# Kernel tuning notes

Hardware: AMD Instinct MI355X
Metric: run time of the kernel (lower is better)

Reference implementation:

```python
import jax, jax.numpy as jnp
import numpy as np

B, T, D = 2, 2048, 1024
H, RANK = 16, 32
DH = D // H  # 64


def setup_inputs() -> dict:
    key = jax.random.key(0)
    ks = jax.random.split(key, 6)
    sd = 1.0 / np.sqrt(D)
    sdh = 1.0 / np.sqrt(DH)
    return {
        "x": jax.random.normal(ks[0], (B, T, D), dtype=jnp.float32),
        "W_qkv": jax.random.normal(ks[1], (D, 3 * D), dtype=jnp.float32) * sd,
        "W_q_lsr": jax.random.normal(ks[2], (H, DH, RANK), dtype=jnp.float32) * sdh,
        "W_k_lsr": jax.random.normal(ks[3], (H, DH, RANK), dtype=jnp.float32) * sdh,
        "lsr_core": jnp.ones((H, RANK), dtype=jnp.float32),
        "W_o": jax.random.normal(ks[4], (D, D), dtype=jnp.float32) * sd,
    }


def reference(x, W_qkv, W_q_lsr, W_k_lsr, lsr_core, W_o):
    b, t, d = x.shape
    # Fused QKV projection
    qkv = x @ W_qkv  # (B, T, 3D)
    q, k, v = jnp.split(qkv, 3, axis=-1)
    # (B, H, T, DH)
    q = q.reshape(b, t, H, DH).transpose(0, 2, 1, 3)
    k = k.reshape(b, t, H, DH).transpose(0, 2, 1, 3)
    v = v.reshape(b, t, H, DH).transpose(0, 2, 1, 3)
    # Low-rank bilinear score: q^T Wq diag(core) Wk^T k
    ql = jnp.einsum("bhtd,hdr->bhtr", q, W_q_lsr)  # (B, H, T, R)
    kl = jnp.einsum("bhsd,hdr->bhsr", k, W_k_lsr)  # (B, H, T, R)
    scale = 1.0 / jnp.sqrt(jnp.asarray(RANK, dtype=x.dtype))
    scores = jnp.einsum("bhtr,bhsr->bhts", ql * lsr_core[None, :, None, :], kl) * scale
    # Causal mask
    causal = jnp.tril(jnp.ones((t, t), dtype=bool))
    scores = jnp.where(causal[None, None], scores, jnp.asarray(-jnp.inf, dtype=scores.dtype))
    attn = jax.nn.softmax(scores, axis=-1)
    y = jnp.einsum("bhts,bhsd->bhtd", attn, v)  # (B, H, T, DH)
    y = y.transpose(0, 2, 1, 3).reshape(b, t, d)
    return y @ W_o
```

## Files before the change

### kernel.cpp

```cpp
#include <hip/hip_runtime.h>
#include <hip/hip_bf16.h>

#define B_  2
#define T_  2048
#define D_  1024
#define H_  16
#define DH_ 64
#define R_  32
#define BT_ (B_*T_)
#define BH_ (B_*H_)

typedef unsigned short u16;
typedef unsigned int   u32;
typedef __attribute__((ext_vector_type(8))) short bhalf8;
typedef __attribute__((ext_vector_type(4))) float floatx4;

#define WSB_FLAG  0
#define WSB_XB    256
#define WSB_WCATT (WSB_XB    + 8388608)
#define WSB_QL    (WSB_WCATT + 4194304)
#define WSB_KL    (WSB_QL    + 4194304)
#define WSB_VT    (WSB_KL    + 4194304)
#define WSB_YB    (WSB_VT    + 8388608)
#define WSB_WOT   (WSB_YB    + 8388608)

#define NEG_ -1.0e30f

__device__ __forceinline__ float bfs(u16 s) {
    union { u32 i; float f; } w; w.i = ((u32)s) << 16; return w.f;
}
__device__ __forceinline__ u16 tob(float f) {
    __hip_bfloat16 h = __float2bfloat16(f);
    return *(u16*)&h;
}
__device__ __forceinline__ u32 pack2(float a, float b) {
    return (u32)tob(a) | ((u32)tob(b) << 16);
}
__device__ __forceinline__ void gload16(const u16* g, u16* l) {
    __builtin_amdgcn_global_load_lds(
        (const __attribute__((address_space(1))) void*)g,
        (__attribute__((address_space(3))) void*)l, 16, 0, 0);
}
__device__ __forceinline__ int detect_isbf(const u32* __restrict__ xw, int lane) {
    int hits = 0;
    #pragma unroll
    for (int i = 0; i < 8; ++i) {
        const u32 w = xw[lane + i * 64];
        const u32 h = w & 0xFFFFu;
        const u32 e = (h >> 7) & 0xFFu;
        if (h == 0u || (e >= 100u && e <= 150u)) ++hits;
    }
    #pragma unroll
    for (int off = 32; off; off >>= 1) hits += __shfl_down(hits, off, 64);
    return __shfl(hits, 0, 64) >= 300;
}

__global__ __launch_bounds__(256) void prep_kernel(
    const void* __restrict__ x, u16* __restrict__ xb,
    const void* __restrict__ Wqkv, const void* __restrict__ Wo,
    const void* __restrict__ Wq_lsr, const void* __restrict__ Wk_lsr,
    const void* __restrict__ core,
    u16* __restrict__ WcatT, u16* __restrict__ WoT)
{
    __shared__ __align__(16) u16 Bq[128 * 72];
    __shared__ __align__(16) u16 Bk[128 * 72];
    __shared__ __align__(16) u16 Aq[32 * 72];
    __shared__ __align__(16) u16 Ak[32 * 72];
    const int tid  = threadIdx.x;
    const int lane = tid & 63;
    const int isbf = detect_isbf((const u32*)x, lane);
    const int blk  = blockIdx.x;
    const int w    = tid >> 6;
    const int n16  = lane & 15;
    const int q4   = lane >> 4;

    if (blk < 2048) {
        const int e = blk * 256 + tid;
        if (isbf) {
            ((uint4*)xb)[e] = ((const uint4*)x)[e];
        } else {
            float4 a0 = ((const float4*)x)[2*e];
            float4 a1 = ((const float4*)x)[2*e + 1];
            uint4 o;
            o.x = pack2(a0.x, a0.y); o.y = pack2(a0.z, a0.w);
            o.z = pack2(a1.x, a1.y); o.w = pack2(a1.z, a1.w);
            ((uint4*)xb)[e] = o;
        }
        return;
    }

    if (blk < 2560) {
        int t = blk - 2048;
        const void* src; u16* dst; int srcStride, srcColOff, dstRowOff;
        if (t < 256) { src = Wqkv; dst = WcatT; srcStride = 3*D_; srcColOff = 2*D_; dstRowOff = 1024; }
        else { t -= 256; src = Wo; dst = WoT; srcStride = D_; srcColOff = 0; dstRowOff = 0; }
        const int j0 = (t & 15) * 64;
        const int i0 = (t >> 4) * 64;
        #pragma unroll
        for (int p = 0; p < 2; ++p) {
            const int e = tid + p * 256;
            const int r = e >> 3, ch = e & 7;
            if (isbf) {
                uint4 v = *(const uint4*)((const u16*)src + (size_t)(i0 + r) * srcStride + srcColOff + j0 + ch*8);
                *(uint4*)&Bq[r * 72 + ch*8] = v;
            } else {
                const float* s = (const float*)src + (size_t)(i0 + r) * srcStride + srcColOff + j0 + ch*8;
                float4 a0 = *(const float4*)s;
                float4 a1 = *(const float4*)(s + 4);
                uint4 o;
                o.x = pack2(a0.x, a0.y); o.y = pack2(a0.z, a0.w);
                o.z = pack2(a1.x, a1.y); o.w = pack2(a1.z, a1.w);
                *(uint4*)&Bq[r * 72 + ch*8] = o;
            }
        }
        __syncthreads();
        #pragma unroll
        for (int p = 0; p < 2; ++p) {
            const int e = tid + p * 256;
            const int c = e >> 3, ch = e & 7;
            u16 tmp[8];
            #pragma unroll
            for (int j = 0; j < 8; ++j) tmp[j] = Bq[(ch*8 + j) * 72 + c];
            *(uint4*)(dst + (size_t)(dstRowOff + j0 + c) * D_ + i0 + ch*8) = *(uint4*)tmp;
        }
        return;
    }

    const int fb = blk - 2560;
    const int h  = fb & 15;
    const int d0 = (fb >> 4) * 128;

    #pragma unroll
    for (int p = 0; p < 8; ++p) {
        const int e  = tid + p * 256;
        const int r  = e & 31, dh = e >> 5;
        float aq, ak;
        if (isbf) {
            aq = bfs(((const u16*)Wq_lsr)[(h*DH_ + dh)*R_ + r]);
            ak = bfs(((const u16*)Wk_lsr)[(h*DH_ + dh)*R_ + r]);
        } else {
            aq = ((const float*)Wq_lsr)[(h*DH_ + dh)*R_ + r];
            ak = ((const float*)Wk_lsr)[(h*DH_ + dh)*R_ + r];
        }
        Aq[r * 72 + dh] = tob(aq);
        Ak[r * 72 + dh] = tob(ak);
    }
    #pragma unroll
    for (int p = 0; p < 8; ++p) {
        const int e  = tid + p * 256;
        const int n  = e >> 4, ch = e & 15;
        if (isbf) {
            uint2 wq = *(const uint2*)((const u16*)Wqkv + (size_t)(d0+n)*(3*D_) + h*DH_ + ch*4);
            uint2 wk = *(const uint2*)((const u16*)Wqkv + (size_t)(d0+n)*(3*D_) + D_ + h*DH_ + ch*4);
            *(uint2*)&Bq[n * 72 + ch*4] = wq;
            *(uint2*)&Bk[n * 72 + ch*4] = wk;
        } else {
            float4 fq = *(const float4*)((const float*)Wqkv + (size_t)(d0+n)*(3*D_) + h*DH_ + ch*4);
            float4 fk = *(const float4*)((const float*)Wqkv + (size_t)(d0+n)*(3*D_) + D_ + h*DH_ + ch*4);
            uint2 oq, ok;
            oq.x = pack2(fq.x, fq.y); oq.y = pack2(fq.z, fq.w);
            ok.x = pack2(fk.x, fk.y); ok.y = pack2(fk.z, fk.w);
            *(uint2*)&Bq[n * 72 + ch*4] = oq;
            *(uint2*)&Bk[n * 72 + ch*4] = ok;
        }
    }
    __syncthreads();

    floatx4 accq[2][2], acck[2][2];
    #pragma unroll
    for (int mi = 0; mi < 2; ++mi)
        #pragma unroll
        for (int ni = 0; ni < 2; ++ni) { accq[mi][ni] = (floatx4)(0.f); acck[mi][ni] = (floatx4)(0.f); }

    #pragma unroll
    for (int kk = 0; kk < 2; ++kk) {
        bhalf8 aqf[2], akf[2], bqf[2], bkf[2];
        #pragma unroll
        for (int mi = 0; mi < 2; ++mi) {
            aqf[mi] = *(const bhalf8*)&Aq[(mi*16 + n16) * 72 + kk*32 + q4*8];
            akf[mi] = *(const bhalf8*)&Ak[(mi*16 + n16) * 72 + kk*32 + q4*8];
        }
        #pragma unroll
        for (int ni = 0; ni < 2; ++ni) {
            bqf[ni] = *(const bhalf8*)&Bq[(w*32 + ni*16 + n16) * 72 + kk*32 + q4*8];
            bkf[ni] = *(const bhalf8*)&Bk[(w*32 + ni*16 + n16) * 72 + kk*32 + q4*8];
        }
        #pragma unroll
        for (int mi = 0; mi < 2; ++mi)
            #pragma unroll
            for (int ni = 0; ni < 2; ++ni) {
                accq[mi][ni] = __builtin_amdgcn_mfma_f32_16x16x32_bf16(aqf[mi], bqf[ni], accq[mi][ni], 0, 0, 0);
                acck[mi][ni] = __builtin_amdgcn_mfma_f32_16x16x32_bf16(akf[mi], bkf[ni], acck[mi][ni], 0, 0, 0);
            }
    }

    const float scale = (float)(0.17677669529663687 * 1.4426950408889634);
    #pragma unroll
    for (int mi = 0; mi < 2; ++mi) {
        #pragma unroll
        for (int rr = 0; rr < 4; ++rr) {
            const int r = mi*16 + q4*4 + rr;
            const float cc = (isbf ? bfs(((const u16*)core)[h*R_ + r])
                                   : ((const float*)core)[h*R_ + r]) * scale;
            #pragma unroll
            for (int ni = 0; ni < 2; ++ni) {
                const int d = d0 + w*32 + ni*16 + n16;
                WcatT[(size_t)(h*R_ + r) * D_ + d]       = tob(accq[mi][ni][rr] * cc);
                WcatT[(size_t)(512 + h*R_ + r) * D_ + d] = tob(acck[mi][ni][rr]);
            }
        }
    }
}

__global__ __launch_bounds__(256, 4) void gemm1_mfma(
    const u16* __restrict__ xb, const u16* __restrict__ WcatT,
    u16* __restrict__ ql, u16* __restrict__ kl, u16* __restrict__ vf)
{
    __shared__ __align__(16) u16 As[128 * 64];
    __shared__ __align__(16) u16 Bs[64 * 64];
    const int tid  = threadIdx.x;
    const int lane = tid & 63;
    const int w    = tid >> 6;
    const int n16  = lane & 15;
    const int q4   = lane >> 4;
    const int wx   = w & 1;
    const int wy   = w >> 1;
    const int bm   = blockIdx.y * 128;
    const int bn   = blockIdx.x * 64;
    const int lrow = lane >> 3;
    const int lcol = (lane & 7) * 8;

    floatx4 acc[4][2];
    #pragma unroll
    for (int i = 0; i < 4; ++i)
        #pragma unroll
        for (int j = 0; j < 2; ++j) acc[i][j] = (floatx4)(0.f);

    for (int kt = 0; kt < D_; kt += 64) {
        #pragma unroll
        for (int i = 0; i < 4; ++i) {
            const int r0 = w*32 + i*8;
            gload16(xb + (size_t)(bm + r0 + lrow) * D_ + kt + lcol, &As[r0 * 64]);
        }
        #pragma unroll
        for (int i = 0; i < 2; ++i) {
            const int r0 = w*16 + i*8;
            gload16(WcatT + (size_t)(bn + r0 + lrow) * D_ + kt + lcol, &Bs[r0 * 64]);
        }
        __syncthreads();
        #pragma unroll
        for (int kk = 0; kk < 2; ++kk) {
            bhalf8 a[4], b[2];
            #pragma unroll
            for (int mi = 0; mi < 4; ++mi)
                a[mi] = *(const bhalf8*)&As[(wy*64 + mi*16 + n16) * 64 + kk*32 + q4*8];
            #pragma unroll
            for (int ni = 0; ni < 2; ++ni)
                b[ni] = *(const bhalf8*)&Bs[(wx*32 + ni*16 + n16) * 64 + kk*32 + q4*8];
            #pragma unroll
            for (int mi = 0; mi < 4; ++mi)
                #pragma unroll
                for (int ni = 0; ni < 2; ++ni)
                    acc[mi][ni] = __builtin_amdgcn_mfma_f32_16x16x32_bf16(
                        a[mi], b[ni], acc[mi][ni], 0, 0, 0);
        }
        __syncthreads();
    }

    if (bn < 1024) {
        #pragma unroll
        for (int mi = 0; mi < 4; ++mi) {
            #pragma unroll
            for (int rr = 0; rr < 4; ++rr) {
                const int row = bm + wy*64 + mi*16 + q4*4 + rr;
                const int b   = row >> 11;
                const int t   = row & (T_ - 1);
                #pragma unroll
                for (int ni = 0; ni < 2; ++ni) {
                    const int col = bn + wx*32 + ni*16 + n16;
                    const u16 val = tob(acc[mi][ni][rr]);
                    if (col < 512) {
                        const int h = col >> 5, r = col & 31;
                        ql[((size_t)(b*H_ + h)*T_ + t)*R_ + r] = val;
                    } else {
                        const int c = col - 512; const int h = c >> 5, r = c & 31;
                        kl[((size_t)(b*H_ + h)*T_ + t)*R_ + r] = val;
                    }
                }
            }
        }
    } else {
        #pragma unroll
        for (int mi = 0; mi < 4; ++mi) {
            const int row0 = bm + wy*64 + mi*16 + q4*4;
            const int b  = row0 >> 11;
            const int t  = row0 & (T_ - 1);
            const int tile = t >> 7;
            const int sl   = t & 127;
            const int kc   = sl >> 5;
            const int j2   = (sl >> 4) & 1;
            const int qv   = (sl >> 2) & 3;
            #pragma unroll
            for (int ni = 0; ni < 2; ++ni) {
                const int c  = bn - 1024 + wx*32 + ni*16 + n16;
                const int h  = c >> 6, dh = c & 63;
                const int bh = b*H_ + h;
                const int c2 = dh >> 4;
                const int lv = qv*16 + (dh & 15);
                u16* dst = vf + ((((size_t)bh*16 + tile)*4 + kc)*4 + c2)*512
                              + lv*8 + j2*4;
                uint2 o;
                o.x = pack2(acc[mi][ni][0], acc[mi][ni][1]);
                o.y = pack2(acc[mi][ni][2], acc[mi][ni][3]);
                *(uint2*)dst = o;
            }
        }
    }
}

__device__ __forceinline__ void softmax_update(
    floatx4 (&Sc)[8], float &mrow, float &lrow, floatx4 (&O)[4], int q4)
{
    float cmax[8];
    #pragma unroll
    for (int c = 0; c < 8; ++c)
        cmax[c] = fmaxf(fmaxf(Sc[c][0], Sc[c][1]), fmaxf(Sc[c][2], Sc[c][3]));
    float rmax = fmaxf(fmaxf(fmaxf(cmax[0], cmax[1]), fmaxf(cmax[2], cmax[3])),
                       fmaxf(fmaxf(cmax[4], cmax[5]), fmaxf(cmax[6], cmax[7])));
    rmax = fmaxf(rmax, __shfl_xor(rmax, 16, 64));
    rmax = fmaxf(rmax, __shfl_xor(rmax, 32, 64));

    const float mn = fmaxf(mrow, rmax);
    const int norescale = __all(rmax <= mrow);

    float csum[8];
    #pragma unroll
    for (int c = 0; c < 8; ++c) {
        #pragma unroll
        for (int r = 0; r < 4; ++r)
            Sc[c][r] = __builtin_amdgcn_exp2f(Sc[c][r] - mn);
        csum[c] = (Sc[c][0] + Sc[c][1]) + (Sc[c][2] + Sc[c][3]);
    }
    float rsum = ((csum[0] + csum[1]) + (csum[2] + csum[3]))
               + ((csum[4] + csum[5]) + (csum[6] + csum[7]));
    rsum += __shfl_xor(rsum, 16, 64);
    rsum += __shfl_xor(rsum, 32, 64);

    if (norescale) {
        lrow += rsum;
    } else {
        const float alpha = __builtin_amdgcn_exp2f(mrow - mn);
        mrow = mn;
        lrow = lrow * alpha + rsum;
        float aO[4];
        #pragma unroll
        for (int r = 0; r < 4; ++r) aO[r] = __shfl(alpha, q4*4 + r, 64);
        #pragma unroll
        for (int c2 = 0; c2 < 4; ++c2)
            #pragma unroll
            for (int r = 0; r < 4; ++r) O[c2][r] *= aO[r];
    }
}

__global__ __launch_bounds__(256, 3) void attn_kernel(
    const u16* __restrict__ ql, const u16* __restrict__ kl,
    const u16* __restrict__ vf, u16* __restrict__ y)
{
    const int tid  = threadIdx.x;
    const int lane = tid & 63;
    const int w    = tid >> 6;
    const int n16  = lane & 15;
    const int q4   = lane >> 4;
    const int task = blockIdx.x * 4 + w;
    const int qt   = 127 - (task >> 5);
    const int bh   = task & 31;
    const int nt   = (qt >> 3) + 1;

    const u16* qlb = ql + (size_t)bh * T_ * R_;
    const u16* klb = kl + (size_t)bh * T_ * R_;
    const u16* vfb = vf + (size_t)bh * 131072;

    const bhalf8 aq = *(const bhalf8*)(qlb + (size_t)(16*qt + n16) * R_ + q4*8);

    float mrow = NEG_, lrow = 0.f;
    floatx4 O[4];
    #pragma unroll
    for (int c = 0; c < 4; ++c) O[c] = (floatx4)(0.f);

    for (int it = 0; it < nt; ++it) {
        const u16* kt = klb + (size_t)(it*128 + n16) * R_ + q4*8;
        floatx4 Sc[8];
        #pragma unroll
        for (int c = 0; c < 8; ++c) {
            bhalf8 ak = *(const bhalf8*)(kt + (size_t)(16*c) * R_);
            Sc[c] = __builtin_amdgcn_mfma_f32_16x16x32_bf16(ak, aq, (floatx4)(0.f), 0, 0, 0);
        }

        if (it == nt - 1) {
            const int tq = 16*(qt & 7) + n16;
            #pragma unroll
            for (int c = 0; c < 8; ++c) {
                const int sb = 16*c + 4*q4;
                #pragma unroll
                for (int r = 0; r < 4; ++r)
                    if (sb + r > tq) Sc[c][r] = NEG_;
            }
        }

        softmax_update(Sc, mrow, lrow, O, q4);

        const u16* vt = vfb + (size_t)it * 8192 + lane*8;
        #pragma unroll
        for (int kc = 0; kc < 4; ++kc) {
            union { u32 wd[4]; bhalf8 v; } pu;
            pu.wd[0] = pack2(Sc[2*kc    ][0], Sc[2*kc    ][1]);
            pu.wd[1] = pack2(Sc[2*kc    ][2], Sc[2*kc    ][3]);
            pu.wd[2] = pack2(Sc[2*kc + 1][0], Sc[2*kc + 1][1]);
            pu.wd[3] = pack2(Sc[2*kc + 1][2], Sc[2*kc + 1][3]);
            const bhalf8 pa = pu.v;
            #pragma unroll
            for (int c2 = 0; c2 < 4; ++c2) {
                bhalf8 bv = *(const bhalf8*)(vt + (size_t)(kc*4 + c2) * 512);
                O[c2] = __builtin_amdgcn_mfma_f32_16x16x32_bf16(pa, bv, O[c2], 0, 0, 0);
            }
        }
    }

    const int b = bh >> 4, h = bh & 15;
    float lb[4];
    #pragma unroll
    for (int r = 0; r < 4; ++r) lb[r] = __shfl(lrow, q4*4 + r, 64);
    #pragma unroll
    for (int r = 0; r < 4; ++r) {
        const float rl = 1.0f / lb[r];
        const int t = 16*qt + q4*4 + r;
        #pragma unroll
        for (int c2 = 0; c2 < 4; ++c2)
            y[((size_t)b * T_ + t) * D_ + h * DH_ + 16*c2 + n16] = tob(O[c2][r] * rl);
    }
}

__global__ __launch_bounds__(256, 4) void out_gemm_mfma(
    const u16* __restrict__ yb, const u16* __restrict__ WoT,
    float* __restrict__ out)
{
    __shared__ __align__(16) u16 As[64 * 64];
    __shared__ __align__(16) u16 Bs[64 * 64];
    const int tid  = threadIdx.x;
    const int lane = tid & 63;
    const int w    = tid >> 6;
    const int n16  = lane & 15;
    const int q4   = lane >> 4;
    const int wx   = w & 1;
    const int wy   = w >> 1;
    const int bm   = blockIdx.y * 64;
    const int bn   = blockIdx.x * 64;
    const int lrow = lane >> 3;
    const int lcol = (lane & 7) * 8;

    floatx4 acc[2][2];
    #pragma unroll
    for (int i = 0; i < 2; ++i)
        #pragma unroll
        for (int j = 0; j < 2; ++j) acc[i][j] = (floatx4)(0.f);

    for (int kt = 0; kt < D_; kt += 64) {
        #pragma unroll
        for (int i = 0; i < 2; ++i) {
            const int r0 = w*16 + i*8;
            gload16(yb  + (size_t)(bm + r0 + lrow) * D_ + kt + lcol, &As[r0 * 64]);
            gload16(WoT + (size_t)(bn + r0 + lrow) * D_ + kt + lcol, &Bs[r0 * 64]);
        }
        __syncthreads();
        #pragma unroll
        for (int kk = 0; kk < 2; ++kk) {
            bhalf8 a[2], b[2];
            #pragma unroll
            for (int mi = 0; mi < 2; ++mi)
                a[mi] = *(const bhalf8*)&As[(wy*32 + mi*16 + n16) * 64 + kk*32 + q4*8];
            #pragma unroll
            for (int ni = 0; ni < 2; ++ni)
                b[ni] = *(const bhalf8*)&Bs[(wx*32 + ni*16 + n16) * 64 + kk*32 + q4*8];
            #pragma unroll
            for (int mi = 0; mi < 2; ++mi)
                #pragma unroll
                for (int ni = 0; ni < 2; ++ni)
                    acc[mi][ni] = __builtin_amdgcn_mfma_f32_16x16x32_bf16(
                        a[mi], b[ni], acc[mi][ni], 0, 0, 0);
        }
        __syncthreads();
    }

    #pragma unroll
    for (int mi = 0; mi < 2; ++mi) {
        #pragma unroll
        for (int rr = 0; rr < 4; ++rr) {
            const int row = bm + wy*32 + mi*16 + q4*4 + rr;
            #pragma unroll
            for (int ni = 0; ni < 2; ++ni) {
                const int col = bn + wx*32 + ni*16 + n16;
                out[(size_t)row * D_ + col] = acc[mi][ni][rr];
            }
        }
    }
}

extern "C" void kernel_launch(void* const* d_in, const int* in_sizes, int n_in,
                              void* d_out, int out_size, void* d_ws, size_t ws_size,
                              hipStream_t stream)
{
    (void)out_size; (void)ws_size;
    const void* in_x = nullptr; const void* in_wqkv = nullptr;
    const void* in_wq = nullptr; const void* in_wk = nullptr;
    const void* in_core = nullptr; const void* in_wo = nullptr;
    for (int i = 0; i < n_in; ++i) {
        const int s = in_sizes[i];
        if      (s == BT_*D_)     { if (!in_x)    in_x    = d_in[i]; }
        else if (s == D_*3*D_)    { if (!in_wqkv) in_wqkv = d_in[i]; }
        else if (s == H_*DH_*R_)  { if (!in_wq)   in_wq   = d_in[i]; else if (!in_wk) in_wk = d_in[i]; }
        else if (s == H_*R_)      { if (!in_core) in_core = d_in[i]; }
        else if (s == D_*D_)      { if (!in_wo)   in_wo   = d_in[i]; }
    }
    if (!in_x)    in_x    = d_in[0];
    if (!in_wqkv) in_wqkv = d_in[1];
    if (!in_wq)   in_wq   = d_in[2];
    if (!in_wk)   in_wk   = d_in[3];
    if (!in_core) in_core = d_in[4];
    if (!in_wo)   in_wo   = d_in[5];

    float* out = (float*)d_out;

    char* ws    = (char*)d_ws;
    u16*  xb    = (u16*)(ws + WSB_XB);
    u16*  WcatT = (u16*)(ws + WSB_WCATT);
    u16*  ql    = (u16*)(ws + WSB_QL);
    u16*  kl    = (u16*)(ws + WSB_KL);
    u16*  vf    = (u16*)(ws + WSB_VT);
    u16*  yb    = (u16*)(ws + WSB_YB);
    u16*  WoT   = (u16*)(ws + WSB_WOT);

    prep_kernel<<<2688, 256, 0, stream>>>(in_x, xb, in_wqkv, in_wo,
                                          in_wq, in_wk, in_core, WcatT, WoT);
    gemm1_mfma<<<dim3(32, 32), 256, 0, stream>>>(xb, WcatT, ql, kl, vf);
    attn_kernel<<<1024, 256, 0, stream>>>(ql, kl, vf, yb);
    out_gemm_mfma<<<dim3(16, 64), 256, 0, stream>>>(yb, WoT, out);
}
```

Baseline: 186.5 us.

## Share K/V tiles in LDS across 8 waves per attention block with prefetch

Attention blocks now hold 8 waves that cover a 128-query tile of one head. The K tile is staged through LDS and V is double-buffered there with asynchronous prefetch of the next tile, so each tile is fetched from global memory once per block rather than once per wave. The PV MFMA operands are swapped so each lane owns one query row, which removes the alpha and l shuffles and allows vectorized output stores. The cost is block-wide syncs every iteration and coarser causal load balance, since there are now 512 blocks of 8 waves.

```diff
diff --git a/kernel.cpp b/kernel.cpp
--- a/kernel.cpp
+++ b/kernel.cpp
@@ -319,7 +319,7 @@
 }
 
 __device__ __forceinline__ void softmax_update(
-    floatx4 (&Sc)[8], float &mrow, float &lrow, floatx4 (&O)[4], int q4)
+    floatx4 (&Sc)[8], float &mrow, float &lrow, floatx4 (&O)[4])
 {
     float cmax[8];
     #pragma unroll
@@ -352,35 +352,42 @@
         const float alpha = __builtin_amdgcn_exp2f(mrow - mn);
         mrow = mn;
         lrow = lrow * alpha + rsum;
-        float aO[4];
-        #pragma unroll
-        for (int r = 0; r < 4; ++r) aO[r] = __shfl(alpha, q4*4 + r, 64);
         #pragma unroll
         for (int c2 = 0; c2 < 4; ++c2)
             #pragma unroll
-            for (int r = 0; r < 4; ++r) O[c2][r] *= aO[r];
-    }
-}
-
-__global__ __launch_bounds__(256, 3) void attn_kernel(
+            for (int r = 0; r < 4; ++r) O[c2][r] *= alpha;
+    }
+}
+
+__global__ __launch_bounds__(512, 4) void attn_kernel(
     const u16* __restrict__ ql, const u16* __restrict__ kl,
     const u16* __restrict__ vf, u16* __restrict__ y)
 {
+    __shared__ __align__(16) u16 kls[128 * 40];
+    __shared__ __align__(16) u16 vsT[2][8192];
+
     const int tid  = threadIdx.x;
     const int lane = tid & 63;
     const int w    = tid >> 6;
     const int n16  = lane & 15;
     const int q4   = lane >> 4;
-    const int task = blockIdx.x * 4 + w;
-    const int qt   = 127 - (task >> 5);
-    const int bh   = task & 31;
-    const int nt   = (qt >> 3) + 1;
+    const int bh   = blockIdx.x;
+    const int by   = blockIdx.y;
+    const int qt2  = (by < 8) ? (15 - by) : (by - 8);
+    const int t0   = qt2 * 128;
+    const int nt   = qt2 + 1;
 
     const u16* qlb = ql + (size_t)bh * T_ * R_;
+    const bhalf8 aq = *(const bhalf8*)(qlb + (size_t)(t0 + w*16 + n16) * R_ + q4*8);
+
     const u16* klb = kl + (size_t)bh * T_ * R_;
     const u16* vfb = vf + (size_t)bh * 131072;
-
-    const bhalf8 aq = *(const bhalf8*)(qlb + (size_t)(16*qt + n16) * R_ + q4*8);
+    const int rk = tid >> 2, ck = (tid & 3) * 8;
+
+    uint4 kc0 = *(const uint4*)(klb + (size_t)rk * R_ + ck);
+    uint4 kn0 = kc0;
+    gload16(vfb + (size_t)(w*2    ) * 512 + lane*8, &vsT[0][(w*2    ) * 512]);
+    gload16(vfb + (size_t)(w*2 + 1) * 512 + lane*8, &vsT[0][(w*2 + 1) * 512]);
 
     float mrow = NEG_, lrow = 0.f;
     floatx4 O[4];
@@ -388,16 +395,26 @@
     for (int c = 0; c < 4; ++c) O[c] = (floatx4)(0.f);
 
     for (int it = 0; it < nt; ++it) {
-        const u16* kt = klb + (size_t)(it*128 + n16) * R_ + q4*8;
+        const int cur = it & 1;
+        __syncthreads();
+        *(uint4*)&kls[rk * 40 + ck] = kc0;
+        __syncthreads();
+        if (it + 1 < nt) {
+            const u16* vnb = vfb + (size_t)(it + 1) * 8192;
+            gload16(vnb + (size_t)(w*2    ) * 512 + lane*8, &vsT[cur ^ 1][(w*2    ) * 512]);
+            gload16(vnb + (size_t)(w*2 + 1) * 512 + lane*8, &vsT[cur ^ 1][(w*2 + 1) * 512]);
+            kn0 = *(const uint4*)(klb + (size_t)((it+1)*128 + rk) * R_ + ck);
+        }
+
         floatx4 Sc[8];
         #pragma unroll
         for (int c = 0; c < 8; ++c) {
-            bhalf8 ak = *(const bhalf8*)(kt + (size_t)(16*c) * R_);
+            bhalf8 ak = *(const bhalf8*)&kls[(16*c + n16) * 40 + q4*8];
             Sc[c] = __builtin_amdgcn_mfma_f32_16x16x32_bf16(ak, aq, (floatx4)(0.f), 0, 0, 0);
         }
 
         if (it == nt - 1) {
-            const int tq = 16*(qt & 7) + n16;
+            const int tq = w*16 + n16;
             #pragma unroll
             for (int c = 0; c < 8; ++c) {
                 const int sb = 16*c + 4*q4;
@@ -407,9 +424,9 @@
             }
         }
 
-        softmax_update(Sc, mrow, lrow, O, q4);
-
-        const u16* vt = vfb + (size_t)it * 8192 + lane*8;
+        softmax_update(Sc, mrow, lrow, O);
+
+        const u16* vt = &vsT[cur][lane * 8];
         #pragma unroll
         for (int kc = 0; kc < 4; ++kc) {
             union { u32 wd[4]; bhalf8 v; } pu;
@@ -421,22 +438,23 @@
             #pragma unroll
             for (int c2 = 0; c2 < 4; ++c2) {
                 bhalf8 bv = *(const bhalf8*)(vt + (size_t)(kc*4 + c2) * 512);
-                O[c2] = __builtin_amdgcn_mfma_f32_16x16x32_bf16(pa, bv, O[c2], 0, 0, 0);
-            }
-        }
+                O[c2] = __builtin_amdgcn_mfma_f32_16x16x32_bf16(bv, pa, O[c2], 0, 0, 0);
+            }
+        }
+
+        kc0 = kn0;
     }
 
     const int b = bh >> 4, h = bh & 15;
-    float lb[4];
-    #pragma unroll
-    for (int r = 0; r < 4; ++r) lb[r] = __shfl(lrow, q4*4 + r, 64);
-    #pragma unroll
-    for (int r = 0; r < 4; ++r) {
-        const float rl = 1.0f / lb[r];
-        const int t = 16*qt + q4*4 + r;
-        #pragma unroll
-        for (int c2 = 0; c2 < 4; ++c2)
-            y[((size_t)b * T_ + t) * D_ + h * DH_ + 16*c2 + n16] = tob(O[c2][r] * rl);
+    const float rl = 1.0f / lrow;
+    const int t = t0 + w*16 + n16;
+    u16* yr = y + ((size_t)b * T_ + t) * D_ + h * DH_;
+    #pragma unroll
+    for (int c2 = 0; c2 < 4; ++c2) {
+        uint2 o;
+        o.x = pack2(O[c2][0] * rl, O[c2][1] * rl);
+        o.y = pack2(O[c2][2] * rl, O[c2][3] * rl);
+        *(uint2*)(yr + 16*c2 + 4*q4) = o;
     }
 }
 
@@ -542,6 +560,6 @@
     prep_kernel<<<2688, 256, 0, stream>>>(in_x, xb, in_wqkv, in_wo,
                                           in_wq, in_wk, in_core, WcatT, WoT);
     gemm1_mfma<<<dim3(32, 32), 256, 0, stream>>>(xb, WcatT, ql, kl, vf);
-    attn_kernel<<<1024, 256, 0, stream>>>(ql, kl, vf, yb);
+    attn_kernel<<<dim3(32, 16), 512, 0, stream>>>(ql, kl, vf, yb);
     out_gemm_mfma<<<dim3(16, 64), 256, 0, stream>>>(yb, WoT, out);
 }
```

New measurement: 176.5 us (median of 2 runs). 1.06x faster.
